# Kernel optimization log

Hardware: AMD Instinct MI355X
Metric: run time of the kernel (lower is better)

## Reference

```python
import jax, jax.numpy as jnp
import numpy as np

N, K, D = 50000, 32, 128


def setup_inputs() -> dict:
    key = jax.random.key(0)
    k1, k2, k3, k4 = jax.random.split(key, 4)
    v_fea = jax.random.normal(k1, (N, D), dtype=jnp.float32)
    t_emb = jax.random.normal(k2, (N, D), dtype=jnp.float32)
    ef = jax.random.randint(k3, (N, K), 0, N, dtype=jnp.int64)
    # nn.Linear(2D, 2D, bias=False) weight, scaled like torch default init
    W = jax.random.normal(k4, (2 * D, 2 * D), dtype=jnp.float32) * (1.0 / np.sqrt(2 * D))
    return {"v_fea": v_fea, "t_emb": t_emb, "ef": ef, "W": W}


def reference(v_fea, t_emb, ef, W):
    # v: gathered neighbor features [N, K, D]
    v = v_fea[ef]
    # q: [N, 2D]; torch Linear applies x @ W.T
    q = jnp.concatenate([v_fea, t_emb], axis=-1)
    wq = q @ W.T                                   # [N, 2D]
    # k: [N, K, 2D]
    k = jnp.concatenate([v, t_emb[ef]], axis=-1)
    # per-edge score: bmm(k, wq[..., None]) -> [N, K]
    r = jnp.einsum("nkd,nd->nk", k, wq)
    r = jax.nn.softmax(r, axis=1)                  # softmax over neighbors
    # weighted sum over neighbors -> [N, D]
    ef_fea = jnp.einsum("nk,nkd->nd", r, v)
    return ef_fea
```

## Files before the change

### kernel.cpp

```cpp
#include <hip/hip_runtime.h>
#include <hip/hip_bf16.h>

#define D     128
#define TWO_D 256
#define KNB   32

typedef __attribute__((ext_vector_type(8))) short    s8;
typedef __attribute__((ext_vector_type(8))) _Float16 h8;
typedef __attribute__((ext_vector_type(2))) _Float16 h2v;
typedef __attribute__((ext_vector_type(4))) float    f4;

__device__ inline unsigned short f2h(float f) {
    return __builtin_bit_cast(unsigned short, (_Float16)f);
}
__device__ inline float h2f(unsigned short u) {
    return (float)__builtin_bit_cast(_Float16, u);
}

union v16u { s8 s; h2v h[4]; };

__device__ inline float dot8(s8 x, s8 w, float acc) {
#if __has_builtin(__builtin_amdgcn_fdot2)
    v16u ux, uw; ux.s = x; uw.s = w;
#pragma unroll
    for (int j = 0; j < 4; ++j)
        acc = __builtin_amdgcn_fdot2(ux.h[j], uw.h[j], acc, false);
#else
#pragma unroll
    for (int j = 0; j < 8; ++j)
        acc = fmaf(h2f((unsigned short)x[j]), h2f((unsigned short)w[j]), acc);
#endif
    return acc;
}

__device__ inline void gl_lds16(const void* g, void* l) {
    __builtin_amdgcn_global_load_lds(
        (const __attribute__((address_space(1))) void*)g,
        (__attribute__((address_space(3))) void*)l, 16, 0, 0);
}

__device__ inline s8 pack8(float4 x, float4 y) {
    s8 q;
    q[0]=(short)f2h(x.x); q[1]=(short)f2h(x.y); q[2]=(short)f2h(x.z); q[3]=(short)f2h(x.w);
    q[4]=(short)f2h(y.x); q[5]=(short)f2h(y.y); q[6]=(short)f2h(y.z); q[7]=(short)f2h(y.w);
    return q;
}

#define BM 128
#define BN 128
#define BK 32
#define LDT 56

__global__ __launch_bounds__(256) void gemm_cast_wq(
    const float* __restrict__ v_fea, const float* __restrict__ t_emb,
    const float* __restrict__ W, unsigned short* __restrict__ wq_h,
    unsigned short* __restrict__ ph, int M)
{
    __shared__ unsigned short As[BM][LDT];
    __shared__ unsigned short Bs[BN][LDT];

    const int tid  = threadIdx.x;
    const int w    = tid >> 6;
    const int lane = tid & 63;
    const int quad = lane >> 4;
    const int l16  = lane & 15;
    const int row0 = blockIdx.x * BM;
    const int i0   = blockIdx.y * BN;
    const bool wr_ph = (blockIdx.y == 0);

    f4 acc[2][8] = {};

    const int srow = tid >> 1;
    const int seg  = tid & 1;
    const int grow_s = row0 + srow;
    int ga = grow_s; if (ga >= M) ga = M - 1;

    for (int kt = 0; kt < TWO_D; kt += BK) {
        const float* srcA = (kt < D) ? v_fea : t_emb;
        const int kb = (kt & (D - 1)) + seg * 16;
        const float* pa = srcA + (size_t)ga * D + kb;
        float4 a0 = *(const float4*)(pa);
        float4 a1 = *(const float4*)(pa + 4);
        float4 a2 = *(const float4*)(pa + 8);
        float4 a3 = *(const float4*)(pa + 12);
        const float* pb = W + (size_t)(i0 + srow) * TWO_D + kt + seg * 16;
        float4 b0 = *(const float4*)(pb);
        float4 b1 = *(const float4*)(pb + 4);
        float4 b2 = *(const float4*)(pb + 8);
        float4 b3 = *(const float4*)(pb + 12);

        s8 A0 = pack8(a0, a1), A1 = pack8(a2, a3);
        if (wr_ph && grow_s < M) {
            *(s8*)(ph + (size_t)grow_s * TWO_D + kt + seg * 16)     = A0;
            *(s8*)(ph + (size_t)grow_s * TWO_D + kt + seg * 16 + 8) = A1;
        }

        __syncthreads();
        *(s8*)&As[srow][seg * 16]     = A0;
        *(s8*)&As[srow][seg * 16 + 8] = A1;
        *(s8*)&Bs[srow][seg * 16]     = pack8(b0, b1);
        *(s8*)&Bs[srow][seg * 16 + 8] = pack8(b2, b3);
        __syncthreads();

        s8 af0 = *(const s8*)&As[w * 32 + l16][quad * 8];
        s8 af1 = *(const s8*)&As[w * 32 + 16 + l16][quad * 8];
#pragma unroll
        for (int nt = 0; nt < 8; ++nt) {
            s8 bf = *(const s8*)&Bs[nt * 16 + l16][quad * 8];
            acc[0][nt] = __builtin_amdgcn_mfma_f32_16x16x32_f16(
                __builtin_bit_cast(h8, af0), __builtin_bit_cast(h8, bf), acc[0][nt], 0, 0, 0);
            acc[1][nt] = __builtin_amdgcn_mfma_f32_16x16x32_f16(
                __builtin_bit_cast(h8, af1), __builtin_bit_cast(h8, bf), acc[1][nt], 0, 0, 0);
        }
    }

#pragma unroll
    for (int mt = 0; mt < 2; ++mt) {
#pragma unroll
        for (int nt = 0; nt < 8; ++nt) {
#pragma unroll
            for (int r = 0; r < 4; ++r) {
                int grow = row0 + w * 32 + mt * 16 + quad * 4 + r;
                if (grow < M)
                    wq_h[(size_t)grow * TWO_D + i0 + nt * 16 + l16] = f2h(acc[mt][nt][r]);
            }
        }
    }
}

__global__ __attribute__((amdgpu_waves_per_eu(5, 6))) __launch_bounds__(256)
void attn_kernel(
    const unsigned short* __restrict__ ph, const int* __restrict__ ef,
    const unsigned short* __restrict__ wq_h, float* __restrict__ outp, int M)
{
    __shared__ char smem[4][8192];

    const int lane = threadIdx.x & 63;
    const int w    = threadIdx.x >> 6;
    const int n    = blockIdx.x * 4 + w;
    if (n >= M) return;

    const int g = lane >> 4;
    const int j = lane & 15;

    const unsigned short* wp = wq_h + (size_t)n * TWO_D + j * 8;
    s8 wqa = *(const s8*)(wp);
    s8 wqb = *(const s8*)(wp + D);

    int eidx = 0;
    if (lane < KNB) eidx = ef[n * KNB + lane];

    char* base = smem[w];
    s8 t8[8];
#pragma unroll
    for (int p = 0; p < 8; ++p) {
        int e = __shfl(eidx, 4 * p + g, 64);
        const char* rp = (const char*)ph + (size_t)e * 512 + j * 16;
        gl_lds16(rp, base + p * 1024);
        t8[p] = *(const s8*)(rp + 256);
    }
    asm volatile("s_waitcnt vmcnt(0)" ::: "memory");
    __builtin_amdgcn_sched_barrier(0);

    float s[8];
#pragma unroll
    for (int p = 0; p < 8; ++p) {
        s8 v8 = *(const s8*)(base + p * 1024 + lane * 16);
        float t = dot8(v8, wqa, 0.f);
        s[p] = dot8(t8[p], wqb, t);
    }

#pragma unroll
    for (int p = 0; p < 8; ++p) {
#pragma unroll
        for (int off = 8; off; off >>= 1) s[p] += __shfl_xor(s[p], off, 64);
    }
    float m = -1e30f;
#pragma unroll
    for (int p = 0; p < 8; ++p) {
        float sb = __shfl_xor(s[p], 16, 64);
        float m2 = fmaxf(s[p], sb);
        float m3 = __shfl_xor(m2, 32, 64);
        m = fmaxf(m, fmaxf(m2, m3));
    }
    float e[8];
    float psum = 0.f;
#pragma unroll
    for (int p = 0; p < 8; ++p) {
        e[p] = __expf(s[p] - m);
        psum += e[p];
    }
    psum += __shfl_xor(psum, 16, 64);
    psum += __shfl_xor(psum, 32, 64);

    float o[8] = {};
#pragma unroll
    for (int p = 0; p < 8; ++p) {
        s8 v8 = *(const s8*)(base + p * 1024 + lane * 16);
        v16u u; u.s = v8;
#pragma unroll
        for (int t = 0; t < 4; ++t) {
            o[2*t]   = fmaf(e[p], (float)u.h[t][0], o[2*t]);
            o[2*t+1] = fmaf(e[p], (float)u.h[t][1], o[2*t+1]);
        }
    }
#pragma unroll
    for (int t = 0; t < 8; ++t) {
        o[t] += __shfl_xor(o[t], 16, 64);
        o[t] += __shfl_xor(o[t], 32, 64);
    }

    if (lane < 16) {
        float inv = 1.0f / psum;
        float* orow = outp + (size_t)n * D + j * 8;
        *(float4*)(orow)     = make_float4(o[0]*inv, o[1]*inv, o[2]*inv, o[3]*inv);
        *(float4*)(orow + 4) = make_float4(o[4]*inv, o[5]*inv, o[6]*inv, o[7]*inv);
    }
}

extern "C" void kernel_launch(void* const* d_in, const int* in_sizes, int n_in,
                              void* d_out, int out_size, void* d_ws, size_t ws_size,
                              hipStream_t stream)
{
    const float* v_fea = (const float*)d_in[0];
    const float* t_emb = (const float*)d_in[1];
    const int*   ef    = (const int*)d_in[2];
    const float* W     = (const float*)d_in[3];
    float* outp = (float*)d_out;

    const int M = in_sizes[0] / D;
    char* ws = (char*)d_ws;
    unsigned short* wq_h = (unsigned short*)ws;
    unsigned short* ph   = (unsigned short*)(ws + (size_t)M * TWO_D * 2);

    dim3 gg((M + BM - 1) / BM, TWO_D / BN);
    gemm_cast_wq<<<gg, 256, 0, stream>>>(v_fea, t_emb, W, wq_h, ph, M);
    attn_kernel<<<(M + 3) / 4, 256, 0, stream>>>(ph, ef, wq_h, outp, M);
}
```

Before: 222.9 us.

## Split fp32-to-fp16 cast into separate kernel and use LDS-free GEMM

Replaces the fused cast+GEMM kernel with a dedicated cast kernel that converts v_fea, t_emb and W to fp16 once, followed by a GEMM that reads fp16 operands straight from global memory into MFMA fragments without shared memory or barriers. Before, the fp32 A tile was loaded and converted twice, once per N-half block, and every k-step paid two __syncthreads. The new path adds an extra launch plus a write and re-read of the fp16 buffer, and relies on cache hits for the uncoalesced fragment loads. W_h falls back to the output buffer if workspace is too small.

```diff
diff --git a/kernel.cpp b/kernel.cpp
--- a/kernel.cpp
+++ b/kernel.cpp
@@ -46,83 +46,76 @@
     return q;
 }
 
-#define BM 128
-#define BN 128
-#define BK 32
-#define LDT 56
-
-__global__ __launch_bounds__(256) void gemm_cast_wq(
-    const float* __restrict__ v_fea, const float* __restrict__ t_emb,
-    const float* __restrict__ W, unsigned short* __restrict__ wq_h,
-    unsigned short* __restrict__ ph, int M)
-{
-    __shared__ unsigned short As[BM][LDT];
-    __shared__ unsigned short Bs[BN][LDT];
-
-    const int tid  = threadIdx.x;
-    const int w    = tid >> 6;
-    const int lane = tid & 63;
+__global__ __launch_bounds__(256) void cast_kernel(
+    const float* __restrict__ a, const float* __restrict__ b,
+    const float* __restrict__ W,
+    unsigned short* __restrict__ ph, unsigned short* __restrict__ W_h,
+    int total)
+{
+    int i = blockIdx.x * 256 + threadIdx.x;
+    if (i < total) {
+        int n = i >> 4, j = i & 15;
+        const float4* pv = (const float4*)(a + (size_t)n * D + j * 8);
+        const float4* pt = (const float4*)(b + (size_t)n * D + j * 8);
+        float4 v0 = pv[0], v1 = pv[1];
+        float4 t0 = pt[0], t1 = pt[1];
+        *(s8*)(ph + (size_t)n * TWO_D + j * 8)     = pack8(v0, v1);
+        *(s8*)(ph + (size_t)n * TWO_D + D + j * 8) = pack8(t0, t1);
+    } else if (i < total + 4096) {
+        int t = i - total;
+        const float4* src = (const float4*)(W + (size_t)t * 16);
+        float4 w0 = src[0], w1 = src[1], w2 = src[2], w3 = src[3];
+        *(s8*)(W_h + (size_t)t * 16)     = pack8(w0, w1);
+        *(s8*)(W_h + (size_t)t * 16 + 8) = pack8(w2, w3);
+    }
+}
+
+__global__ __launch_bounds__(256) void gemm_wq(
+    const unsigned short* __restrict__ ph, const unsigned short* __restrict__ W_h,
+    unsigned short* __restrict__ wq_h, int M)
+{
+    const int w    = threadIdx.x >> 6;
+    const int lane = threadIdx.x & 63;
     const int quad = lane >> 4;
     const int l16  = lane & 15;
-    const int row0 = blockIdx.x * BM;
-    const int i0   = blockIdx.y * BN;
-    const bool wr_ph = (blockIdx.y == 0);
+
+    const int wid = blockIdx.x * 4 + w;
+    const int mg  = wid >> 1;
+    const int m0  = mg * 32;
+    if (m0 >= M) return;
+    const int n0  = (wid & 1) * 128;
 
     f4 acc[2][8] = {};
 
-    const int srow = tid >> 1;
-    const int seg  = tid & 1;
-    const int grow_s = row0 + srow;
-    int ga = grow_s; if (ga >= M) ga = M - 1;
-
-    for (int kt = 0; kt < TWO_D; kt += BK) {
-        const float* srcA = (kt < D) ? v_fea : t_emb;
-        const int kb = (kt & (D - 1)) + seg * 16;
-        const float* pa = srcA + (size_t)ga * D + kb;
-        float4 a0 = *(const float4*)(pa);
-        float4 a1 = *(const float4*)(pa + 4);
-        float4 a2 = *(const float4*)(pa + 8);
-        float4 a3 = *(const float4*)(pa + 12);
-        const float* pb = W + (size_t)(i0 + srow) * TWO_D + kt + seg * 16;
-        float4 b0 = *(const float4*)(pb);
-        float4 b1 = *(const float4*)(pb + 4);
-        float4 b2 = *(const float4*)(pb + 8);
-        float4 b3 = *(const float4*)(pb + 12);
-
-        s8 A0 = pack8(a0, a1), A1 = pack8(a2, a3);
-        if (wr_ph && grow_s < M) {
-            *(s8*)(ph + (size_t)grow_s * TWO_D + kt + seg * 16)     = A0;
-            *(s8*)(ph + (size_t)grow_s * TWO_D + kt + seg * 16 + 8) = A1;
+    int ra0 = m0 + l16;      if (ra0 >= M) ra0 = M - 1;
+    int ra1 = m0 + 16 + l16; if (ra1 >= M) ra1 = M - 1;
+    const unsigned short* pa0 = ph  + (size_t)ra0 * TWO_D + quad * 8;
+    const unsigned short* pa1 = ph  + (size_t)ra1 * TWO_D + quad * 8;
+    const unsigned short* pb  = W_h + (size_t)(n0 + l16) * TWO_D + quad * 8;
+
+#pragma unroll 2
+    for (int kt = 0; kt < 8; ++kt) {
+        s8 a0 = *(const s8*)(pa0 + kt * 32);
+        s8 a1 = *(const s8*)(pa1 + kt * 32);
+#pragma unroll
+        for (int nt = 0; nt < 8; ++nt) {
+            s8 bf = *(const s8*)(pb + (size_t)nt * 16 * TWO_D + kt * 32);
+            acc[0][nt] = __builtin_amdgcn_mfma_f32_16x16x32_f16(
+                __builtin_bit_cast(h8, a0), __builtin_bit_cast(h8, bf), acc[0][nt], 0, 0, 0);
+            acc[1][nt] = __builtin_amdgcn_mfma_f32_16x16x32_f16(
+                __builtin_bit_cast(h8, a1), __builtin_bit_cast(h8, bf), acc[1][nt], 0, 0, 0);
         }
-
-        __syncthreads();
-        *(s8*)&As[srow][seg * 16]     = A0;
-        *(s8*)&As[srow][seg * 16 + 8] = A1;
-        *(s8*)&Bs[srow][seg * 16]     = pack8(b0, b1);
-        *(s8*)&Bs[srow][seg * 16 + 8] = pack8(b2, b3);
-        __syncthreads();
-
-        s8 af0 = *(const s8*)&As[w * 32 + l16][quad * 8];
-        s8 af1 = *(const s8*)&As[w * 32 + 16 + l16][quad * 8];
+    }
+
+#pragma unroll
+    for (int mt = 0; mt < 2; ++mt) {
 #pragma unroll
         for (int nt = 0; nt < 8; ++nt) {
-            s8 bf = *(const s8*)&Bs[nt * 16 + l16][quad * 8];
-            acc[0][nt] = __builtin_amdgcn_mfma_f32_16x16x32_f16(
-                __builtin_bit_cast(h8, af0), __builtin_bit_cast(h8, bf), acc[0][nt], 0, 0, 0);
-            acc[1][nt] = __builtin_amdgcn_mfma_f32_16x16x32_f16(
-                __builtin_bit_cast(h8, af1), __builtin_bit_cast(h8, bf), acc[1][nt], 0, 0, 0);
-        }
-    }
-
-#pragma unroll
-    for (int mt = 0; mt < 2; ++mt) {
-#pragma unroll
-        for (int nt = 0; nt < 8; ++nt) {
 #pragma unroll
             for (int r = 0; r < 4; ++r) {
-                int grow = row0 + w * 32 + mt * 16 + quad * 4 + r;
+                int grow = m0 + mt * 16 + quad * 4 + r;
                 if (grow < M)
-                    wq_h[(size_t)grow * TWO_D + i0 + nt * 16 + l16] = f2h(acc[mt][nt][r]);
+                    wq_h[(size_t)grow * TWO_D + n0 + nt * 16 + l16] = f2h(acc[mt][nt][r]);
             }
         }
     }
@@ -232,8 +225,17 @@
     char* ws = (char*)d_ws;
     unsigned short* wq_h = (unsigned short*)ws;
     unsigned short* ph   = (unsigned short*)(ws + (size_t)M * TWO_D * 2);
-
-    dim3 gg((M + BM - 1) / BM, TWO_D / BN);
-    gemm_cast_wq<<<gg, 256, 0, stream>>>(v_fea, t_emb, W, wq_h, ph, M);
+    size_t used = (size_t)M * TWO_D * 2 * 2;
+    unsigned short* W_h = (ws_size >= used + 131072)
+                              ? (unsigned short*)(ws + used)
+                              : (unsigned short*)d_out;
+
+    const int total = M * 16;
+    cast_kernel<<<(total + 4096 + 255) / 256, 256, 0, stream>>>(
+        v_fea, t_emb, W, ph, W_h, total);
+
+    const int nwaves = 2 * ((M + 31) / 32);
+    gemm_wq<<<(nwaves + 3) / 4, 256, 0, stream>>>(ph, W_h, wq_h, M);
+
     attn_kernel<<<(M + 3) / 4, 256, 0, stream>>>(ph, ef, wq_h, outp, M);
 }
```

Measured after the change: 242.2 us. 8.6% more time.
